# Performance work log

Measured on AMD Instinct MI355X. Metric: run time of the kernel, lower is better.

Reference implementation:

```python
import jax, jax.numpy as jnp
import numpy as np

N = 50000      # nodes
E = 1600000    # edges (avg degree 32)
R = 8          # relation types
G = 64         # graphs in batch
D_IN = 128
HID = 128
CLS = 10


def setup_inputs() -> dict:
    key = jax.random.key(0)
    ks = jax.random.split(key, 12)
    s = 0.05  # weight init scale
    return {
        "x": jax.random.normal(ks[0], (N, D_IN), dtype=jnp.float32),
        "edge_index": jax.random.randint(ks[1], (2, E), 0, N, dtype=jnp.int32),
        "edge_type": jax.random.randint(ks[2], (E,), 0, R, dtype=jnp.int32),
        "batch": jnp.sort(jax.random.randint(ks[3], (N,), 0, G, dtype=jnp.int32)),
        "W1": jax.random.normal(ks[4], (R, D_IN, HID), dtype=jnp.float32) * s,
        "root1": jax.random.normal(ks[5], (D_IN, HID), dtype=jnp.float32) * s,
        "b1": jax.random.normal(ks[6], (HID,), dtype=jnp.float32) * s,
        "W2": jax.random.normal(ks[7], (R, HID, HID), dtype=jnp.float32) * s,
        "root2": jax.random.normal(ks[8], (HID, HID), dtype=jnp.float32) * s,
        "b2": jax.random.normal(ks[9], (HID,), dtype=jnp.float32) * s,
        "lin_w": jax.random.normal(ks[10], (HID, CLS), dtype=jnp.float32) * s,
        "lin_b": jax.random.normal(ks[11], (CLS,), dtype=jnp.float32) * s,
    }


def rgcn_conv(x, edge_index, edge_type, W, root, bias):
    # PyG RGCNConv (default aggr='mean'): per-relation mean of neighbor
    # features, relation-specific matmul, summed over relations, + root + bias.
    src, dst = edge_index[0], edge_index[1]
    d_in = x.shape[1]
    seg = dst * R + edge_type                      # fused (node, relation) segment id
    msg = jax.ops.segment_sum(x[src], seg, num_segments=N * R)          # [N*R, d_in]
    cnt = jax.ops.segment_sum(jnp.ones((E,), x.dtype), seg, num_segments=N * R)
    mean = (msg / jnp.maximum(cnt, 1.0)[:, None]).reshape(N, R, d_in)   # [N, R, d_in]
    return jnp.einsum('nrd,rdh->nh', mean, W) + x @ root + bias


def reference(x, edge_index, edge_type, batch, W1, root1, b1, W2, root2, b2, lin_w, lin_b):
    h = jax.nn.relu(rgcn_conv(x, edge_index, edge_type, W1, root1, b1))
    h = jax.nn.relu(rgcn_conv(h, edge_index, edge_type, W2, root2, b2))
    # global mean pool per graph
    gsum = jax.ops.segment_sum(h, batch, num_segments=G)                # [G, HID]
    gcnt = jax.ops.segment_sum(jnp.ones((N,), h.dtype), batch, num_segments=G)
    g = gsum / jnp.maximum(gcnt, 1.0)[:, None]
    return g @ lin_w + lin_b                                            # [G, CLS]
```

## Files before the change

kernel.cpp:

```cpp
#include <hip/hip_runtime.h>

#define N_NODES 50000
#define N_EDGES 1600000
#define R_REL 8
#define G_GRAPHS 64
#define D_INF 128
#define HIDF 128
#define CLSF 10

#define S_SEG (N_NODES * R_REL)
#define RZ 9
#define PCHUNK 16

#define XG 8
#define NODES_PER_G (N_NODES / XG)
#define SORT_BLKS_PER_G 256
#define SORT_GRID (XG * SORT_BLKS_PER_G)

typedef __attribute__((ext_vector_type(8))) short short8;
typedef __attribute__((ext_vector_type(4))) float floatx4;

typedef __attribute__((address_space(1))) const unsigned int guint;
typedef __attribute__((address_space(3))) unsigned int luint;
__device__ __forceinline__ void gload_lds16(const void* g, void* l) {
    __builtin_amdgcn_global_load_lds((guint*)g, (luint*)l, 16, 0, 0);
}

__device__ __forceinline__ unsigned short f2bf(float f) {
    unsigned int u = __float_as_uint(f);
    unsigned int r = (u + 0x7fffu + ((u >> 16) & 1u)) >> 16;
    return (unsigned short)r;
}
__device__ __forceinline__ float bflo(unsigned int u) { return __uint_as_float(u << 16); }
__device__ __forceinline__ float bfhi(unsigned int u) { return __uint_as_float(u & 0xffff0000u); }

__global__ __launch_bounds__(256) void count_kernel(const int* __restrict__ dst,
                                                    const int* __restrict__ et,
                                                    int* __restrict__ cnt) {
    int xg = blockIdx.x & (XG - 1);
    int inner = blockIdx.x >> 3;
    int lo = xg * NODES_PER_G, hi = lo + NODES_PER_G;
    for (int e = inner * 256 + threadIdx.x; e < N_EDGES; e += SORT_BLKS_PER_G * 256) {
        int d = dst[e];
        if (d >= lo && d < hi) {
            atomicAdd(&cnt[d * R_REL + et[e]], 1);
        }
    }
}

#define SCAN_BLK 256
#define SCAN_ELEMS 1024
#define NB_SCAN ((S_SEG + SCAN_ELEMS - 1) / SCAN_ELEMS)

__global__ __launch_bounds__(SCAN_BLK) void scan1_kernel(const int* __restrict__ cnt,
                                                         int* __restrict__ off,
                                                         int* __restrict__ bsum) {
    __shared__ int sd[SCAN_BLK];
    int t = threadIdx.x;
    int base = blockIdx.x * SCAN_ELEMS + t * 4;
    int v[4];
    int tsum = 0;
#pragma unroll
    for (int j = 0; j < 4; j++) {
        v[j] = (base + j < S_SEG) ? cnt[base + j] : 0;
        tsum += v[j];
    }
    sd[t] = tsum;
    __syncthreads();
    for (int d = 1; d < SCAN_BLK; d <<= 1) {
        int x = (t >= d) ? sd[t - d] : 0;
        __syncthreads();
        sd[t] += x;
        __syncthreads();
    }
    int incl = sd[t];
    int run = incl - tsum;
#pragma unroll
    for (int j = 0; j < 4; j++) {
        if (base + j < S_SEG) off[base + j] = run;
        run += v[j];
    }
    if (t == SCAN_BLK - 1) bsum[blockIdx.x] = incl;
}

__global__ __launch_bounds__(512) void scan2_kernel(int* __restrict__ bsum) {
    __shared__ int sd[512];
    int t = threadIdx.x;
    int v = (t < NB_SCAN) ? bsum[t] : 0;
    sd[t] = v;
    __syncthreads();
    for (int d = 1; d < 512; d <<= 1) {
        int x = (t >= d) ? sd[t - d] : 0;
        __syncthreads();
        sd[t] += x;
        __syncthreads();
    }
    if (t < NB_SCAN) bsum[t] = sd[t] - v;
}

__global__ void absoff_kernel(int* __restrict__ off, const int* __restrict__ bsum,
                              const int* __restrict__ cnt, float* __restrict__ winv) {
    int i = blockIdx.x * blockDim.x + threadIdx.x;
    if (i < S_SEG) {
        off[i] += bsum[i >> 10];
        winv[i] = 1.0f / (float)max(cnt[i], 1);
    }
}

__global__ __launch_bounds__(256) void bin_kernel(const int* __restrict__ src,
                                                  const int* __restrict__ dst,
                                                  const int* __restrict__ et,
                                                  const float* __restrict__ winv,
                                                  int* __restrict__ cursor,
                                                  int2* __restrict__ zw) {
    int xg = blockIdx.x & (XG - 1);
    int inner = blockIdx.x >> 3;
    int lo = xg * NODES_PER_G, hi = lo + NODES_PER_G;
    for (int e = inner * 256 + threadIdx.x; e < N_EDGES; e += SORT_BLKS_PER_G * 256) {
        int d = dst[e];
        if (d >= lo && d < hi) {
            int t = et[e];
            int seg = d * R_REL + t;
            int pos = atomicAdd(&cursor[seg], 1);
            zw[pos] = make_int2((src[e] * RZ + t) << 7, __float_as_int(winv[seg]));
        }
    }
}

__global__ void convx_kernel(const float* __restrict__ x, unsigned short* __restrict__ xb) {
    int idx = blockIdx.x * blockDim.x + threadIdx.x;
    if (idx < N_NODES * D_INF) xb[idx] = f2bf(x[idx]);
}

__global__ __launch_bounds__(256) void convw9_kernel(const float* __restrict__ W,
                                                     const float* __restrict__ root,
                                                     unsigned short* __restrict__ wz) {
    __shared__ float t[16][17];
    int r = blockIdx.z;
    int k0 = blockIdx.x * 16, c0 = blockIdx.y * 16;
    int tx = threadIdx.x & 15, ty = threadIdx.x >> 4;
    const float* srcp = (r < 8) ? (W + (size_t)r * 128 * 128) : root;
    t[ty][tx] = srcp[(size_t)(k0 + ty) * 128 + c0 + tx];
    __syncthreads();
    wz[(size_t)r * 16384 + (size_t)(c0 + ty) * 128 + k0 + tx] = f2bf(t[tx][ty]);
}

__global__ __launch_bounds__(256) void transform_gemm(
    const unsigned short* __restrict__ hb,
    const unsigned short* __restrict__ wz,
    unsigned short* __restrict__ z)
{
    __shared__ __align__(16) unsigned short A4[4][128][32];
    __shared__ __align__(16) unsigned short Bc[128][32];

    const int tx = threadIdx.x;
    const int wave = tx >> 6, lane = tx & 63;
    const int quad = lane >> 4, lq = lane & 15;
    const int row0 = blockIdx.x * 128;
    const int srow = lane >> 2;
    const int sch  = lane & 3;

#pragma unroll
    for (int kk = 0; kk < 4; kk++) {
#pragma unroll
        for (int p = 0; p < 2; p++) {
            int rr = (wave * 2 + p) * 16;
            int gr = row0 + rr + srow; if (gr >= N_NODES) gr = N_NODES - 1;
            gload_lds16(hb + (size_t)gr * HIDF + kk * 32 + sch * 8, &A4[kk][rr][0]);
        }
    }

    floatx4 acc[2][8];
    for (int r = 0; r < RZ; r++) {
#pragma unroll
        for (int i = 0; i < 2; i++)
#pragma unroll
            for (int j = 0; j < 8; j++) acc[i][j] = (floatx4){0.f, 0.f, 0.f, 0.f};

#pragma unroll
        for (int kk = 0; kk < 4; kk++) {
#pragma unroll
            for (int p = 0; p < 2; p++) {
                int cc = (wave * 2 + p) * 16;
                int gc = cc + srow;
                gload_lds16(wz + ((size_t)r * 128 + gc) * 128 + kk * 32 + sch * 8,
                            &Bc[cc][0]);
            }
            __syncthreads();

            short8 af[2], bfr[8];
#pragma unroll
            for (int i = 0; i < 2; i++)
                af[i] = *(const short8*)(&A4[kk][wave * 32 + i * 16 + lq][quad * 8]);
#pragma unroll
            for (int j = 0; j < 8; j++)
                bfr[j] = *(const short8*)(&Bc[j * 16 + lq][quad * 8]);
#pragma unroll
            for (int i = 0; i < 2; i++)
#pragma unroll
                for (int j = 0; j < 8; j++)
                    acc[i][j] = __builtin_amdgcn_mfma_f32_16x16x32_bf16(af[i], bfr[j], acc[i][j], 0, 0, 0);
            __syncthreads();
        }

#pragma unroll
        for (int i = 0; i < 2; i++) {
#pragma unroll
            for (int j = 0; j < 8; j++) {
                int col = j * 16 + lq;
#pragma unroll
                for (int rg = 0; rg < 4; rg++) {
                    int row = row0 + wave * 32 + i * 16 + quad * 4 + rg;
                    if (row < N_NODES)
                        z[((size_t)row * RZ + r) * 128 + col] = f2bf(acc[i][j][rg]);
                }
            }
        }
    }
}

__global__ __launch_bounds__(256) void agg2_kernel(const unsigned short* __restrict__ z,
                                                   const int2* __restrict__ zw,
                                                   const int* __restrict__ off,
                                                   const float* __restrict__ bias,
                                                   unsigned short* __restrict__ hout) {
    int nod = blockIdx.x * 8 + (threadIdx.x >> 5);
    if (nod >= N_NODES) return;
    int c = threadIdx.x & 31;
    int beg = off[nod * R_REL];
    int end = (nod < N_NODES - 1) ? off[(nod + 1) * R_REL] : N_EDGES;

    float a0 = 0.f, a1 = 0.f, a2 = 0.f, a3 = 0.f;
    int e = beg;
    for (; e + 4 <= end; e += 4) {
        int2 r0 = zw[e + 0], r1 = zw[e + 1], r2 = zw[e + 2], r3 = zw[e + 3];
        float w0 = __int_as_float(r0.y), w1 = __int_as_float(r1.y);
        float w2 = __int_as_float(r2.y), w3 = __int_as_float(r3.y);
        uint2 v0 = *(const uint2*)(z + (size_t)r0.x + c * 4);
        uint2 v1 = *(const uint2*)(z + (size_t)r1.x + c * 4);
        uint2 v2 = *(const uint2*)(z + (size_t)r2.x + c * 4);
        uint2 v3 = *(const uint2*)(z + (size_t)r3.x + c * 4);
        a0 += bflo(v0.x) * w0 + bflo(v1.x) * w1 + bflo(v2.x) * w2 + bflo(v3.x) * w3;
        a1 += bfhi(v0.x) * w0 + bfhi(v1.x) * w1 + bfhi(v2.x) * w2 + bfhi(v3.x) * w3;
        a2 += bflo(v0.y) * w0 + bflo(v1.y) * w1 + bflo(v2.y) * w2 + bflo(v3.y) * w3;
        a3 += bfhi(v0.y) * w0 + bfhi(v1.y) * w1 + bfhi(v2.y) * w2 + bfhi(v3.y) * w3;
    }
    for (; e < end; e++) {
        int2 rr = zw[e];
        float w = __int_as_float(rr.y);
        uint2 v = *(const uint2*)(z + (size_t)rr.x + c * 4);
        a0 += bflo(v.x) * w; a1 += bfhi(v.x) * w;
        a2 += bflo(v.y) * w; a3 += bfhi(v.y) * w;
    }
    uint2 vr = *(const uint2*)(z + ((size_t)nod * RZ + 8) * 128 + c * 4);
    a0 += bflo(vr.x); a1 += bfhi(vr.x); a2 += bflo(vr.y); a3 += bfhi(vr.y);
    float4 b = *(const float4*)(bias + c * 4);
    a0 = fmaxf(a0 + b.x, 0.0f);
    a1 = fmaxf(a1 + b.y, 0.0f);
    a2 = fmaxf(a2 + b.z, 0.0f);
    a3 = fmaxf(a3 + b.w, 0.0f);
    uint2 o;
    o.x = (unsigned int)f2bf(a0) | ((unsigned int)f2bf(a1) << 16);
    o.y = (unsigned int)f2bf(a2) | ((unsigned int)f2bf(a3) << 16);
    *(uint2*)(hout + (size_t)nod * HIDF + c * 4) = o;
}

__global__ __launch_bounds__(256) void pool1_kernel(const unsigned short* __restrict__ h,
                                                    const int* __restrict__ batch,
                                                    float* __restrict__ partial) {
    int g = blockIdx.x;
    int p = blockIdx.y;
    int lo, hi;
    {
        int l = 0, r = N_NODES;
        while (l < r) { int m = (l + r) >> 1; if (batch[m] < g) l = m + 1; else r = m; }
        lo = l;
        l = lo; r = N_NODES;
        while (l < r) { int m = (l + r) >> 1; if (batch[m] < g + 1) l = m + 1; else r = m; }
        hi = l;
    }
    int t = threadIdx.x;
    int rowlane = t >> 5;
    int c4 = t & 31;
    float a0 = 0.f, a1 = 0.f, a2 = 0.f, a3 = 0.f;
    for (int n = lo + p + rowlane * PCHUNK; n < hi; n += 8 * PCHUNK) {
        uint2 v = *(const uint2*)(h + (size_t)n * HIDF + c4 * 4);
        a0 += bflo(v.x); a1 += bfhi(v.x); a2 += bflo(v.y); a3 += bfhi(v.y);
    }
    __shared__ float red[8][128];
    if (rowlane == 0) {
        red[0][c4 * 4 + 0] = a0; red[0][c4 * 4 + 1] = a1;
        red[0][c4 * 4 + 2] = a2; red[0][c4 * 4 + 3] = a3;
    }
    __syncthreads();
    for (int s = 1; s < 8; s++) {
        if (rowlane == s) {
            red[0][c4 * 4 + 0] += a0; red[0][c4 * 4 + 1] += a1;
            red[0][c4 * 4 + 2] += a2; red[0][c4 * 4 + 3] += a3;
        }
        __syncthreads();
    }
    if (t < 128) partial[((size_t)g * PCHUNK + p) * 128 + t] = red[0][t];
}

__global__ __launch_bounds__(128) void pool2_kernel(const float* __restrict__ partial,
                                                    const int* __restrict__ batch,
                                                    float* __restrict__ gmean) {
    int g = blockIdx.x;
    int lo, hi;
    {
        int l = 0, r = N_NODES;
        while (l < r) { int m = (l + r) >> 1; if (batch[m] < g) l = m + 1; else r = m; }
        lo = l;
        l = lo; r = N_NODES;
        while (l < r) { int m = (l + r) >> 1; if (batch[m] < g + 1) l = m + 1; else r = m; }
        hi = l;
    }
    int t = threadIdx.x;
    float s = 0.f;
#pragma unroll
    for (int p = 0; p < PCHUNK; p++)
        s += partial[((size_t)g * PCHUNK + p) * 128 + t];
    gmean[g * HIDF + t] = s / (float)max(hi - lo, 1);
}

__global__ void final_kernel(const float* __restrict__ gmean,
                             const float* __restrict__ lin_w,
                             const float* __restrict__ lin_b,
                             float* __restrict__ out) {
    __shared__ float gl[HIDF];
    int g = blockIdx.x;
    int hh = threadIdx.x;
    gl[hh] = gmean[g * HIDF + hh];
    __syncthreads();
    if (hh < CLSF) {
        float s = lin_b[hh];
#pragma unroll 16
        for (int d = 0; d < HIDF; d++) s += gl[d] * lin_w[d * CLSF + hh];
        out[g * CLSF + hh] = s;
    }
}

extern "C" void kernel_launch(void* const* d_in, const int* in_sizes, int n_in,
                              void* d_out, int out_size, void* d_ws, size_t ws_size,
                              hipStream_t stream) {
    const float* x     = (const float*)d_in[0];
    const int*   ei    = (const int*)d_in[1];
    const int*   et    = (const int*)d_in[2];
    const int*   batch = (const int*)d_in[3];
    const float* W1    = (const float*)d_in[4];
    const float* root1 = (const float*)d_in[5];
    const float* b1    = (const float*)d_in[6];
    const float* W2    = (const float*)d_in[7];
    const float* root2 = (const float*)d_in[8];
    const float* b2    = (const float*)d_in[9];
    const float* lin_w = (const float*)d_in[10];
    const float* lin_b = (const float*)d_in[11];
    float* out = (float*)d_out;

    const int* src = ei;
    const int* dst = ei + N_EDGES;

    char* ws = (char*)d_ws;
    unsigned short* xb  = (unsigned short*)ws; ws += (size_t)N_NODES * HIDF * 2;
    unsigned short* h1  = (unsigned short*)ws; ws += (size_t)N_NODES * HIDF * 2;
    unsigned short* h2  = (unsigned short*)ws; ws += (size_t)N_NODES * HIDF * 2;
    unsigned short* z   = (unsigned short*)ws; ws += (size_t)N_NODES * RZ * 128 * 2;
    unsigned short* wz1 = (unsigned short*)ws; ws += (size_t)RZ * 128 * 128 * 2;
    unsigned short* wz2 = (unsigned short*)ws; ws += (size_t)RZ * 128 * 128 * 2;
    int*   cnt    = (int*)ws;   ws += (size_t)S_SEG * 4;
    int*   off    = (int*)ws;   ws += (size_t)S_SEG * 4;
    int*   bsum   = (int*)ws;   ws += 512 * 4;
    int*   cursor = (int*)ws;   ws += (size_t)S_SEG * 4;
    float* winv   = (float*)ws; ws += (size_t)S_SEG * 4;
    int2*  zw     = (int2*)ws;  ws += (size_t)N_EDGES * 8;
    float* partial = (float*)ws; ws += (size_t)G_GRAPHS * PCHUNK * 128 * 4;
    float* gmean  = (float*)ws; ws += (size_t)G_GRAPHS * HIDF * 4;

    hipMemsetAsync(cnt, 0, (size_t)S_SEG * 4, stream);

    count_kernel<<<SORT_GRID, 256, 0, stream>>>(dst, et, cnt);
    scan1_kernel<<<NB_SCAN, SCAN_BLK, 0, stream>>>(cnt, off, bsum);
    scan2_kernel<<<1, 512, 0, stream>>>(bsum);
    absoff_kernel<<<(S_SEG + 255) / 256, 256, 0, stream>>>(off, bsum, cnt, winv);
    hipMemcpyAsync(cursor, off, (size_t)S_SEG * 4, hipMemcpyDeviceToDevice, stream);
    bin_kernel<<<SORT_GRID, 256, 0, stream>>>(src, dst, et, winv, cursor, zw);

    convx_kernel<<<(N_NODES * D_INF + 255) / 256, 256, 0, stream>>>(x, xb);
    convw9_kernel<<<dim3(8, 8, RZ), 256, 0, stream>>>(W1, root1, wz1);
    convw9_kernel<<<dim3(8, 8, RZ), 256, 0, stream>>>(W2, root2, wz2);

    const int NGB = (N_NODES + 127) / 128;
    const int NAB = (N_NODES + 7) / 8;

    transform_gemm<<<NGB, 256, 0, stream>>>(xb, wz1, z);
    agg2_kernel<<<NAB, 256, 0, stream>>>(z, zw, off, b1, h1);

    transform_gemm<<<NGB, 256, 0, stream>>>(h1, wz2, z);
    agg2_kernel<<<NAB, 256, 0, stream>>>(z, zw, off, b2, h2);

    pool1_kernel<<<dim3(G_GRAPHS, PCHUNK), 256, 0, stream>>>(h2, batch, partial);
    pool2_kernel<<<G_GRAPHS, 128, 0, stream>>>(partial, batch, gmean);
    final_kernel<<<G_GRAPHS, HIDF, 0, stream>>>(gmean, lin_w, lin_b, out);

    (void)in_sizes; (void)n_in; (void)out_size; (void)ws_size;
}
```

Measured before the change: 490.8 us.

## Fuse aggregation and transform into one layer kernel, aggregate-then-transform order

Replaces the transform-then-aggregate scheme, which wrote a 9x-expanded per-relation z tensor and gathered from it, with one fused kernel per layer. That kernel gathers the neighbour mean per relation into shared memory, multiplies it by that relation's weights with MFMA, and adds the root term, bias and ReLU at the end. This removes the large z buffer write and read and halves the per-edge gather record, since only the source id is stored. It also precomputes segment ids once, so counting and binning read a single array with nontemporal loads. The trade-off is that the gather now happens inside the GEMM kernel with low occupancy (128 nodes per block, serial relations), so gather latency may be hidden poorly.

```diff
diff --git a/kernel.cpp b/kernel.cpp
--- a/kernel.cpp
+++ b/kernel.cpp
@@ -34,17 +34,22 @@
 __device__ __forceinline__ float bflo(unsigned int u) { return __uint_as_float(u << 16); }
 __device__ __forceinline__ float bfhi(unsigned int u) { return __uint_as_float(u & 0xffff0000u); }
 
-__global__ __launch_bounds__(256) void count_kernel(const int* __restrict__ dst,
-                                                    const int* __restrict__ et,
+__device__ __forceinline__ int ntload(const int* p) { return __builtin_nontemporal_load(p); }
+
+__global__ void seg_kernel(const int* __restrict__ dst, const int* __restrict__ et,
+                           int* __restrict__ seg) {
+    int e = blockIdx.x * blockDim.x + threadIdx.x;
+    if (e < N_EDGES) seg[e] = dst[e] * R_REL + et[e];
+}
+
+__global__ __launch_bounds__(256) void count_kernel(const int* __restrict__ seg,
                                                     int* __restrict__ cnt) {
     int xg = blockIdx.x & (XG - 1);
     int inner = blockIdx.x >> 3;
-    int lo = xg * NODES_PER_G, hi = lo + NODES_PER_G;
+    int lo = xg * NODES_PER_G * R_REL, hi = lo + NODES_PER_G * R_REL;
     for (int e = inner * 256 + threadIdx.x; e < N_EDGES; e += SORT_BLKS_PER_G * 256) {
-        int d = dst[e];
-        if (d >= lo && d < hi) {
-            atomicAdd(&cnt[d * R_REL + et[e]], 1);
-        }
+        int sg = ntload(seg + e);
+        if (sg >= lo && sg < hi) atomicAdd(&cnt[sg], 1);
     }
 }
 
@@ -107,22 +112,18 @@
     }
 }
 
-__global__ __launch_bounds__(256) void bin_kernel(const int* __restrict__ src,
-                                                  const int* __restrict__ dst,
-                                                  const int* __restrict__ et,
-                                                  const float* __restrict__ winv,
+__global__ __launch_bounds__(256) void bin_kernel(const int* __restrict__ seg,
+                                                  const int* __restrict__ src,
                                                   int* __restrict__ cursor,
-                                                  int2* __restrict__ zw) {
+                                                  int* __restrict__ esrc) {
     int xg = blockIdx.x & (XG - 1);
     int inner = blockIdx.x >> 3;
-    int lo = xg * NODES_PER_G, hi = lo + NODES_PER_G;
+    int lo = xg * NODES_PER_G * R_REL, hi = lo + NODES_PER_G * R_REL;
     for (int e = inner * 256 + threadIdx.x; e < N_EDGES; e += SORT_BLKS_PER_G * 256) {
-        int d = dst[e];
-        if (d >= lo && d < hi) {
-            int t = et[e];
-            int seg = d * R_REL + t;
-            int pos = atomicAdd(&cursor[seg], 1);
-            zw[pos] = make_int2((src[e] * RZ + t) << 7, __float_as_int(winv[seg]));
+        int sg = ntload(seg + e);
+        if (sg >= lo && sg < hi) {
+            int pos = atomicAdd(&cursor[sg], 1);
+            esrc[pos] = ntload(src + e);
         }
     }
 }
@@ -145,124 +146,134 @@
     wz[(size_t)r * 16384 + (size_t)(c0 + ty) * 128 + k0 + tx] = f2bf(t[tx][ty]);
 }
 
-__global__ __launch_bounds__(256) void transform_gemm(
-    const unsigned short* __restrict__ hb,
+__global__ __launch_bounds__(256) void fused_layer(
+    const unsigned short* __restrict__ hsrc,
     const unsigned short* __restrict__ wz,
-    unsigned short* __restrict__ z)
+    const int* __restrict__ esrc,
+    const int* __restrict__ off,
+    const float* __restrict__ winv,
+    const float* __restrict__ bias,
+    unsigned short* __restrict__ hout)
 {
-    __shared__ __align__(16) unsigned short A4[4][128][32];
-    __shared__ __align__(16) unsigned short Bc[128][32];
+    __shared__ __align__(16) unsigned short M[4][128][32];
+    __shared__ __align__(16) unsigned short B4[4][128][32];
 
     const int tx = threadIdx.x;
     const int wave = tx >> 6, lane = tx & 63;
     const int quad = lane >> 4, lq = lane & 15;
+    const int srow = lane >> 2, sch = lane & 3;
     const int row0 = blockIdx.x * 128;
-    const int srow = lane >> 2;
-    const int sch  = lane & 3;
-
-#pragma unroll
-    for (int kk = 0; kk < 4; kk++) {
+    const int grp = tx >> 5;
+    const int c4 = tx & 31;
+
+    floatx4 acc[2][8];
+#pragma unroll
+    for (int i = 0; i < 2; i++)
+#pragma unroll
+        for (int j = 0; j < 8; j++) acc[i][j] = (floatx4){0.f, 0.f, 0.f, 0.f};
+
+    for (int r = 0; r < R_REL; r++) {
+#pragma unroll
+        for (int kk = 0; kk < 4; kk++)
+#pragma unroll
+            for (int p = 0; p < 2; p++) {
+                int cc = (wave * 2 + p) * 16;
+                gload_lds16(wz + ((size_t)r * 128 + cc + srow) * 128 + kk * 32 + sch * 8,
+                            &B4[kk][cc][0]);
+            }
+
+        for (int it = 0; it < 16; it++) {
+            int nloc = grp * 16 + it;
+            int node = row0 + nloc;
+            float a0 = 0.f, a1 = 0.f, a2 = 0.f, a3 = 0.f;
+            if (node < N_NODES) {
+                int sg = node * R_REL + r;
+                int beg = off[sg];
+                int end = (sg + 1 < S_SEG) ? off[sg + 1] : N_EDGES;
+                float w = winv[sg];
+                int e = beg;
+                for (; e + 2 <= end; e += 2) {
+                    int s0 = esrc[e], s1 = esrc[e + 1];
+                    uint2 v0 = *(const uint2*)(hsrc + (size_t)s0 * HIDF + c4 * 4);
+                    uint2 v1 = *(const uint2*)(hsrc + (size_t)s1 * HIDF + c4 * 4);
+                    a0 += bflo(v0.x) + bflo(v1.x);
+                    a1 += bfhi(v0.x) + bfhi(v1.x);
+                    a2 += bflo(v0.y) + bflo(v1.y);
+                    a3 += bfhi(v0.y) + bfhi(v1.y);
+                }
+                if (e < end) {
+                    int s0 = esrc[e];
+                    uint2 v0 = *(const uint2*)(hsrc + (size_t)s0 * HIDF + c4 * 4);
+                    a0 += bflo(v0.x); a1 += bfhi(v0.x);
+                    a2 += bflo(v0.y); a3 += bfhi(v0.y);
+                }
+                a0 *= w; a1 *= w; a2 *= w; a3 *= w;
+            }
+            uint2 o;
+            o.x = (unsigned int)f2bf(a0) | ((unsigned int)f2bf(a1) << 16);
+            o.y = (unsigned int)f2bf(a2) | ((unsigned int)f2bf(a3) << 16);
+            *(uint2*)&M[c4 >> 3][nloc][(c4 & 7) * 4] = o;
+        }
+        __syncthreads();
+
+#pragma unroll
+        for (int kk = 0; kk < 4; kk++) {
+            short8 af[2], bfr[8];
+#pragma unroll
+            for (int i = 0; i < 2; i++)
+                af[i] = *(const short8*)(&M[kk][wave * 32 + i * 16 + lq][quad * 8]);
+#pragma unroll
+            for (int j = 0; j < 8; j++)
+                bfr[j] = *(const short8*)(&B4[kk][j * 16 + lq][quad * 8]);
+#pragma unroll
+            for (int i = 0; i < 2; i++)
+#pragma unroll
+                for (int j = 0; j < 8; j++)
+                    acc[i][j] = __builtin_amdgcn_mfma_f32_16x16x32_bf16(af[i], bfr[j], acc[i][j], 0, 0, 0);
+        }
+        __syncthreads();
+    }
+
+#pragma unroll
+    for (int kk = 0; kk < 4; kk++)
 #pragma unroll
         for (int p = 0; p < 2; p++) {
             int rr = (wave * 2 + p) * 16;
             int gr = row0 + rr + srow; if (gr >= N_NODES) gr = N_NODES - 1;
-            gload_lds16(hb + (size_t)gr * HIDF + kk * 32 + sch * 8, &A4[kk][rr][0]);
-        }
-    }
-
-    floatx4 acc[2][8];
-    for (int r = 0; r < RZ; r++) {
+            gload_lds16(hsrc + (size_t)gr * HIDF + kk * 32 + sch * 8, &M[kk][rr][0]);
+            gload_lds16(wz + ((size_t)8 * 128 + rr + srow) * 128 + kk * 32 + sch * 8,
+                        &B4[kk][rr][0]);
+        }
+    __syncthreads();
+#pragma unroll
+    for (int kk = 0; kk < 4; kk++) {
+        short8 af[2], bfr[8];
 #pragma unroll
         for (int i = 0; i < 2; i++)
-#pragma unroll
-            for (int j = 0; j < 8; j++) acc[i][j] = (floatx4){0.f, 0.f, 0.f, 0.f};
-
-#pragma unroll
-        for (int kk = 0; kk < 4; kk++) {
-#pragma unroll
-            for (int p = 0; p < 2; p++) {
-                int cc = (wave * 2 + p) * 16;
-                int gc = cc + srow;
-                gload_lds16(wz + ((size_t)r * 128 + gc) * 128 + kk * 32 + sch * 8,
-                            &Bc[cc][0]);
+            af[i] = *(const short8*)(&M[kk][wave * 32 + i * 16 + lq][quad * 8]);
+#pragma unroll
+        for (int j = 0; j < 8; j++)
+            bfr[j] = *(const short8*)(&B4[kk][j * 16 + lq][quad * 8]);
+#pragma unroll
+        for (int i = 0; i < 2; i++)
+#pragma unroll
+            for (int j = 0; j < 8; j++)
+                acc[i][j] = __builtin_amdgcn_mfma_f32_16x16x32_bf16(af[i], bfr[j], acc[i][j], 0, 0, 0);
+    }
+
+#pragma unroll
+    for (int i = 0; i < 2; i++)
+#pragma unroll
+        for (int j = 0; j < 8; j++) {
+            int col = j * 16 + lq;
+            float bv = bias[col];
+#pragma unroll
+            for (int rg = 0; rg < 4; rg++) {
+                int row = row0 + wave * 32 + i * 16 + quad * 4 + rg;
+                if (row < N_NODES)
+                    hout[(size_t)row * HIDF + col] = f2bf(fmaxf(acc[i][j][rg] + bv, 0.f));
             }
-            __syncthreads();
-
-            short8 af[2], bfr[8];
-#pragma unroll
-            for (int i = 0; i < 2; i++)
-                af[i] = *(const short8*)(&A4[kk][wave * 32 + i * 16 + lq][quad * 8]);
-#pragma unroll
-            for (int j = 0; j < 8; j++)
-                bfr[j] = *(const short8*)(&Bc[j * 16 + lq][quad * 8]);
-#pragma unroll
-            for (int i = 0; i < 2; i++)
-#pragma unroll
-                for (int j = 0; j < 8; j++)
-                    acc[i][j] = __builtin_amdgcn_mfma_f32_16x16x32_bf16(af[i], bfr[j], acc[i][j], 0, 0, 0);
-            __syncthreads();
-        }
-
-#pragma unroll
-        for (int i = 0; i < 2; i++) {
-#pragma unroll
-            for (int j = 0; j < 8; j++) {
-                int col = j * 16 + lq;
-#pragma unroll
-                for (int rg = 0; rg < 4; rg++) {
-                    int row = row0 + wave * 32 + i * 16 + quad * 4 + rg;
-                    if (row < N_NODES)
-                        z[((size_t)row * RZ + r) * 128 + col] = f2bf(acc[i][j][rg]);
-                }
-            }
-        }
-    }
-}
-
-__global__ __launch_bounds__(256) void agg2_kernel(const unsigned short* __restrict__ z,
-                                                   const int2* __restrict__ zw,
-                                                   const int* __restrict__ off,
-                                                   const float* __restrict__ bias,
-                                                   unsigned short* __restrict__ hout) {
-    int nod = blockIdx.x * 8 + (threadIdx.x >> 5);
-    if (nod >= N_NODES) return;
-    int c = threadIdx.x & 31;
-    int beg = off[nod * R_REL];
-    int end = (nod < N_NODES - 1) ? off[(nod + 1) * R_REL] : N_EDGES;
-
-    float a0 = 0.f, a1 = 0.f, a2 = 0.f, a3 = 0.f;
-    int e = beg;
-    for (; e + 4 <= end; e += 4) {
-        int2 r0 = zw[e + 0], r1 = zw[e + 1], r2 = zw[e + 2], r3 = zw[e + 3];
-        float w0 = __int_as_float(r0.y), w1 = __int_as_float(r1.y);
-        float w2 = __int_as_float(r2.y), w3 = __int_as_float(r3.y);
-        uint2 v0 = *(const uint2*)(z + (size_t)r0.x + c * 4);
-        uint2 v1 = *(const uint2*)(z + (size_t)r1.x + c * 4);
-        uint2 v2 = *(const uint2*)(z + (size_t)r2.x + c * 4);
-        uint2 v3 = *(const uint2*)(z + (size_t)r3.x + c * 4);
-        a0 += bflo(v0.x) * w0 + bflo(v1.x) * w1 + bflo(v2.x) * w2 + bflo(v3.x) * w3;
-        a1 += bfhi(v0.x) * w0 + bfhi(v1.x) * w1 + bfhi(v2.x) * w2 + bfhi(v3.x) * w3;
-        a2 += bflo(v0.y) * w0 + bflo(v1.y) * w1 + bflo(v2.y) * w2 + bflo(v3.y) * w3;
-        a3 += bfhi(v0.y) * w0 + bfhi(v1.y) * w1 + bfhi(v2.y) * w2 + bfhi(v3.y) * w3;
-    }
-    for (; e < end; e++) {
-        int2 rr = zw[e];
-        float w = __int_as_float(rr.y);
-        uint2 v = *(const uint2*)(z + (size_t)rr.x + c * 4);
-        a0 += bflo(v.x) * w; a1 += bfhi(v.x) * w;
-        a2 += bflo(v.y) * w; a3 += bfhi(v.y) * w;
-    }
-    uint2 vr = *(const uint2*)(z + ((size_t)nod * RZ + 8) * 128 + c * 4);
-    a0 += bflo(vr.x); a1 += bfhi(vr.x); a2 += bflo(vr.y); a3 += bfhi(vr.y);
-    float4 b = *(const float4*)(bias + c * 4);
-    a0 = fmaxf(a0 + b.x, 0.0f);
-    a1 = fmaxf(a1 + b.y, 0.0f);
-    a2 = fmaxf(a2 + b.z, 0.0f);
-    a3 = fmaxf(a3 + b.w, 0.0f);
-    uint2 o;
-    o.x = (unsigned int)f2bf(a0) | ((unsigned int)f2bf(a1) << 16);
-    o.y = (unsigned int)f2bf(a2) | ((unsigned int)f2bf(a3) << 16);
-    *(uint2*)(hout + (size_t)nod * HIDF + c * 4) = o;
+        }
 }
 
 __global__ __launch_bounds__(256) void pool1_kernel(const unsigned short* __restrict__ h,
@@ -365,39 +376,36 @@
     unsigned short* xb  = (unsigned short*)ws; ws += (size_t)N_NODES * HIDF * 2;
     unsigned short* h1  = (unsigned short*)ws; ws += (size_t)N_NODES * HIDF * 2;
     unsigned short* h2  = (unsigned short*)ws; ws += (size_t)N_NODES * HIDF * 2;
-    unsigned short* z   = (unsigned short*)ws; ws += (size_t)N_NODES * RZ * 128 * 2;
     unsigned short* wz1 = (unsigned short*)ws; ws += (size_t)RZ * 128 * 128 * 2;
     unsigned short* wz2 = (unsigned short*)ws; ws += (size_t)RZ * 128 * 128 * 2;
+    int*   seg    = (int*)ws;   ws += (size_t)N_EDGES * 4;
     int*   cnt    = (int*)ws;   ws += (size_t)S_SEG * 4;
     int*   off    = (int*)ws;   ws += (size_t)S_SEG * 4;
     int*   bsum   = (int*)ws;   ws += 512 * 4;
     int*   cursor = (int*)ws;   ws += (size_t)S_SEG * 4;
     float* winv   = (float*)ws; ws += (size_t)S_SEG * 4;
-    int2*  zw     = (int2*)ws;  ws += (size_t)N_EDGES * 8;
+    int*   esrc   = (int*)ws;   ws += (size_t)N_EDGES * 4;
     float* partial = (float*)ws; ws += (size_t)G_GRAPHS * PCHUNK * 128 * 4;
     float* gmean  = (float*)ws; ws += (size_t)G_GRAPHS * HIDF * 4;
 
     hipMemsetAsync(cnt, 0, (size_t)S_SEG * 4, stream);
 
-    count_kernel<<<SORT_GRID, 256, 0, stream>>>(dst, et, cnt);
+    seg_kernel<<<(N_EDGES + 255) / 256, 256, 0, stream>>>(dst, et, seg);
+    count_kernel<<<SORT_GRID, 256, 0, stream>>>(seg, cnt);
     scan1_kernel<<<NB_SCAN, SCAN_BLK, 0, stream>>>(cnt, off, bsum);
     scan2_kernel<<<1, 512, 0, stream>>>(bsum);
     absoff_kernel<<<(S_SEG + 255) / 256, 256, 0, stream>>>(off, bsum, cnt, winv);
     hipMemcpyAsync(cursor, off, (size_t)S_SEG * 4, hipMemcpyDeviceToDevice, stream);
-    bin_kernel<<<SORT_GRID, 256, 0, stream>>>(src, dst, et, winv, cursor, zw);
+    bin_kernel<<<SORT_GRID, 256, 0, stream>>>(seg, src, cursor, esrc);
 
     convx_kernel<<<(N_NODES * D_INF + 255) / 256, 256, 0, stream>>>(x, xb);
     convw9_kernel<<<dim3(8, 8, RZ), 256, 0, stream>>>(W1, root1, wz1);
     convw9_kernel<<<dim3(8, 8, RZ), 256, 0, stream>>>(W2, root2, wz2);
 
     const int NGB = (N_NODES + 127) / 128;
-    const int NAB = (N_NODES + 7) / 8;
-
-    transform_gemm<<<NGB, 256, 0, stream>>>(xb, wz1, z);
-    agg2_kernel<<<NAB, 256, 0, stream>>>(z, zw, off, b1, h1);
-
-    transform_gemm<<<NGB, 256, 0, stream>>>(h1, wz2, z);
-    agg2_kernel<<<NAB, 256, 0, stream>>>(z, zw, off, b2, h2);
+
+    fused_layer<<<NGB, 256, 0, stream>>>(xb, wz1, esrc, off, winv, b1, h1);
+    fused_layer<<<NGB, 256, 0, stream>>>(h1, wz2, esrc, off, winv, b2, h2);
 
     pool1_kernel<<<dim3(G_GRAPHS, PCHUNK), 256, 0, stream>>>(h2, batch, partial);
     pool2_kernel<<<G_GRAPHS, 128, 0, stream>>>(partial, batch, gmean);
```

Result: slower. 953.9 us (+94.3%).
